# Kernel optimization log

Hardware: AMD Instinct MI355X
Metric: run time of the kernel (lower is better)

## Reference

```python
import jax, jax.numpy as jnp
import numpy as np

B, T, D = 2, 2048, 1024
N, K, H = 16, 8, 128  # q heads, kv heads, head_dim
G = N // K            # GQA group size
EPS = 1e-6
THETA = 1000000.0
SCALE = H ** -0.5
K_MASK = float(np.finfo(np.float32).min)


def rms_norm(x, scale):
    # RMSNorm over head_dim (last axis), computed in fp32 like the original
    dtype = x.dtype
    rms = jnp.sqrt(jnp.mean(x.astype(jnp.float32) ** 2, axis=-1, keepdims=True) + EPS)
    return (scale * x / rms).astype(dtype)


def positions_from_segment_ids(seg):
    t = jnp.arange(seg.shape[1], dtype=jnp.int32)[None, :]
    off = jnp.argmax(seg, axis=1, keepdims=True).astype(jnp.int32)
    rel = t - off
    return jnp.where(seg != 0, rel, jnp.int32(2 ** 30))


def rope_sin_cos(positions):
    frac = jnp.arange(0, H, 2, dtype=jnp.float32) / H
    inv_freq = 1.0 / (THETA ** frac)                    # [H/2]
    ang = positions.astype(jnp.float32)[..., None] * inv_freq  # [B,T,H/2]
    return jnp.sin(ang), jnp.cos(ang)


def apply_rope(x, sin, cos):
    # x: [B,T,heads,H]; sin/cos: [B,T,H/2]
    x1, x2 = x[..., : H // 2], x[..., H // 2:]
    s, c = sin[:, :, None, :], cos[:, :, None, :]
    return jnp.concatenate([x1 * c - x2 * s, x2 * c + x1 * s], axis=-1).astype(x.dtype)


def setup_inputs() -> dict:
    key = jax.random.key(0)
    ks = jax.random.split(key, 8)
    std = 0.02
    return {
        "x": jax.random.normal(ks[0], (B, T, D), dtype=jnp.float32),
        "segment_ids": jnp.ones((B, T), dtype=jnp.int32),
        "wq": jax.random.normal(ks[1], (D, N, H), dtype=jnp.float32) * std,
        "wk": jax.random.normal(ks[2], (D, K, H), dtype=jnp.float32) * std,
        "wv": jax.random.normal(ks[3], (D, K, H), dtype=jnp.float32) * std,
        "wo": jax.random.normal(ks[4], (N, H, D), dtype=jnp.float32) * std,
        "q_scale": jnp.ones((H,), dtype=jnp.float32),
        "k_scale": jnp.ones((H,), dtype=jnp.float32),
    }


def reference(x, segment_ids, wq, wk, wv, wo, q_scale, k_scale):
    # QKV projections + QK RMSNorm
    q = rms_norm(jnp.einsum('BTD,DNH->BTNH', x, wq), q_scale)  # [B,T,N,H]
    k = rms_norm(jnp.einsum('BSD,DKH->BSKH', x, wk), k_scale)  # [B,T,K,H]
    v = jnp.einsum('BSD,DKH->BSKH', x, wv)                     # [B,T,K,H]

    # RoPE using segment-relative positions
    pos = positions_from_segment_ids(segment_ids)  # [B,T] int32
    sin, cos = rope_sin_cos(pos)
    q = apply_rope(q, sin, cos)
    k = apply_rope(k, sin, cos)

    # GQA attention: [B,T,K,G,H] x [B,S,K,H] -> [B,T,S,K,G]
    qg = q.reshape(B, T, K, G, H)
    logits = jnp.einsum('BTKGH,BSKH->BTSKG', qg, k) * SCALE

    causal = pos[:, None, :] <= pos[:, :, None]                       # [B,T,S]
    segm = segment_ids[:, None, :] == segment_ids[:, :, None]         # [B,T,S]
    mask = (causal & segm)[:, :, :, None, None]
    logits = jnp.where(mask, logits, K_MASK)

    w = jax.nn.softmax(logits.astype(jnp.float32), axis=2).astype(logits.dtype)
    out = jnp.einsum('BTSKG,BSKH->BTKGH', w, v).reshape(B, T, N, H)
    return jnp.einsum('BTNH,NHD->BTD', out, wo)
```

## Files before the change

### kernel.cpp

```cpp
#include <hip/hip_runtime.h>
#include <hip/hip_bf16.h>


typedef unsigned short u16;
typedef __attribute__((ext_vector_type(8))) short s16x8;
typedef __attribute__((ext_vector_type(4))) float fp32x4;
typedef __attribute__((ext_vector_type(4))) u16 u16x4;

#define MFMA_BF16(a, b, c) __builtin_amdgcn_mfma_f32_16x16x32_bf16((a), (b), (c), 0, 0, 0)

static constexpr int Bq = 2, Tq = 2048, Dq = 1024, NHq = 16, KHq = 8, Hq = 128;
static constexpr float EPSq = 1e-6f;
static constexpr float S2q = 0.08838834764831845f * 1.4426950408889634f;
static constexpr float MAXq = 20.0f;
static constexpr float NEGHUGE = -3.0e38f;

__device__ __forceinline__ u16 f2b(float f) {
  __hip_bfloat16 h = __float2bfloat16(f);
  return *reinterpret_cast<u16*>(&h);
}

__device__ __forceinline__ void gload16(const u16* g, u16* lds_base) {
  __builtin_amdgcn_global_load_lds(
      (const __attribute__((address_space(1))) unsigned int*)(const void*)g,
      (__attribute__((address_space(3))) unsigned int*)(void*)lds_base, 16, 0, 0);
}


__global__ __launch_bounds__(256) void prep_kernel(
    const float* __restrict__ x, const float* __restrict__ wq,
    const float* __restrict__ wk, const float* __restrict__ wv,
    const float* __restrict__ wo, const int* __restrict__ seg,
    u16* __restrict__ xb, u16* __restrict__ wqkv_t, u16* __restrict__ wo_t,
    int* __restrict__ pos) {
  const int bid = blockIdx.x;
  const int tid = threadIdx.x;
  if (bid < 4096) {
    const int i = bid * 1024 + tid * 4;
    const float4 v = *reinterpret_cast<const float4*>(x + i);
    u16x4 o;
    o.x = f2b(v.x); o.y = f2b(v.y); o.z = f2b(v.z); o.w = f2b(v.w);
    *reinterpret_cast<u16x4*>(xb + i) = o;
    return;
  }
  __shared__ float tile[32][33];
  __shared__ int sv[256], si[256];
  const int tx = tid & 31, ty = tid >> 5;
  if (bid < 8192) {
    const int z = bid - 4096;
    const int r0 = (z & 31) * 32;
    const int c0 = (z >> 5) * 32;
    const float* src;
    int stride, coff;
    if (c0 < 2048)      { src = wq; stride = 2048; coff = c0; }
    else if (c0 < 3072) { src = wk; stride = 1024; coff = c0 - 2048; }
    else                { src = wv; stride = 1024; coff = c0 - 3072; }
#pragma unroll
    for (int j = 0; j < 32; j += 8)
      tile[ty + j][tx] = src[(long)(r0 + ty + j) * stride + (coff + tx)];
    __syncthreads();
#pragma unroll
    for (int j = 0; j < 32; j += 8)
      wqkv_t[(long)(c0 + ty + j) * 1024 + (r0 + tx)] = f2b(tile[tx][ty + j]);
    return;
  }
  if (bid < 10240) {
    const int z = bid - 8192;
    const int c0 = (z & 31) * 32;
    const int r0 = (z >> 5) * 32;
#pragma unroll
    for (int j = 0; j < 32; j += 8)
      tile[ty + j][tx] = wo[(long)(r0 + ty + j) * 1024 + (c0 + tx)];
    __syncthreads();
#pragma unroll
    for (int j = 0; j < 32; j += 8)
      wo_t[(long)(c0 + ty + j) * 2048 + (r0 + tx)] = f2b(tile[tx][ty + j]);
    return;
  }
  const int b = bid - 10240;
  const int* s = seg + b * Tq;
  int bestv = -2147483647 - 1, besti = 0x7fffffff;
  for (int t = tid; t < Tq; t += 256) {
    int v = s[t];
    if (v > bestv) { bestv = v; besti = t; }
  }
  sv[tid] = bestv; si[tid] = besti;
  __syncthreads();
  for (int k = 128; k > 0; k >>= 1) {
    if (tid < k) {
      int v2 = sv[tid + k], i2 = si[tid + k];
      if (v2 > sv[tid] || (v2 == sv[tid] && i2 < si[tid])) {
        sv[tid] = v2; si[tid] = i2;
      }
    }
    __syncthreads();
  }
  const int off = si[0];
  for (int t = tid; t < Tq; t += 256)
    pos[b * Tq + t] = (s[t] != 0) ? (t - off) : (1 << 30);
}


__global__ __launch_bounds__(256) void gemm_qkv_kernel(
    const u16* __restrict__ A, const u16* __restrict__ Bt,
    u16* __restrict__ qkv, u16* __restrict__ vt, const int* __restrict__ pos,
    const float* __restrict__ q_scale, const float* __restrict__ k_scale) {
  __shared__ __align__(16) u16 As[128][64];
  __shared__ __align__(16) u16 Bs[128][64];
  const int tid = threadIdx.x;
  const int wave = tid >> 6, lane = tid & 63;
  const int quad = lane >> 4, l16 = lane & 15;
  const int m0 = blockIdx.y * 128, n0 = blockIdx.x * 128;
  const int row8 = lane >> 3;
  const int cgl = (lane & 7) ^ row8;

  const fp32x4 z4 = {0.f, 0.f, 0.f, 0.f};
  fp32x4 acc[2][8];
#pragma unroll
  for (int i = 0; i < 2; ++i)
#pragma unroll
    for (int j = 0; j < 8; ++j) acc[i][j] = z4;

  for (int k0 = 0; k0 < 1024; k0 += 64) {
    __syncthreads();
#pragma unroll
    for (int jj = 0; jj < 4; ++jj) {
      const int R = wave * 32 + jj * 8;
      gload16(A + (size_t)(m0 + R + row8) * 1024 + k0 + cgl * 8, &As[R][0]);
      gload16(Bt + (size_t)(n0 + R + row8) * 1024 + k0 + cgl * 8, &Bs[R][0]);
    }
    __syncthreads();
#pragma unroll
    for (int kh = 0; kh < 2; ++kh) {
      s16x8 af[2], bfr[8];
#pragma unroll
      for (int i = 0; i < 2; ++i)
        af[i] = *(const s16x8*)&As[wave * 32 + i * 16 + l16]
                               [((((kh << 2) | quad) ^ (l16 & 7)) << 3)];
#pragma unroll
      for (int j = 0; j < 8; ++j)
        bfr[j] = *(const s16x8*)&Bs[j * 16 + l16]
                                [((((kh << 2) | quad) ^ (l16 & 7)) << 3)];
#pragma unroll
      for (int i = 0; i < 2; ++i)
#pragma unroll
        for (int j = 0; j < 8; ++j) acc[i][j] = MFMA_BF16(af[i], bfr[j], acc[i][j]);
    }
  }

  const int wrow = m0 + wave * 32;
  if (n0 >= 3072) {
    const int kv8 = (n0 - 3072) >> 7;
    const int bq = wrow >> 11;
    const size_t vbase = (size_t)(bq * KHq + kv8) * Hq * Tq;
#pragma unroll
    for (int i = 0; i < 2; ++i) {
      const int t = (wrow + i * 16 + quad * 4) & 2047;
#pragma unroll
      for (int j = 0; j < 8; ++j) {
        const int h = j * 16 + l16;
        u16x4 o;
#pragma unroll
        for (int r = 0; r < 4; ++r) o[r] = f2b(acc[i][j][r]);
        *reinterpret_cast<u16x4*>(&vt[vbase + (size_t)h * Tq + t]) = o;
      }
    }
    return;
  }
  const float* scp = (n0 < 2048) ? q_scale : k_scale;
  float scl[8];
#pragma unroll
  for (int j = 0; j < 8; ++j) scl[j] = scp[j * 16 + l16];
  float invf[4];
#pragma unroll
  for (int jf = 0; jf < 4; ++jf)
    invf[jf] = __builtin_amdgcn_exp2f(
                   -(float)(jf * 16 + l16) * (19.931568569324174f / 64.0f)) *
               0.15915494309189535f;
#pragma unroll
  for (int i = 0; i < 2; ++i) {
    float ss[4] = {0.f, 0.f, 0.f, 0.f};
#pragma unroll
    for (int j = 0; j < 8; ++j)
#pragma unroll
      for (int r = 0; r < 4; ++r) ss[r] += acc[i][j][r] * acc[i][j][r];
#pragma unroll
    for (int d = 1; d < 16; d <<= 1)
#pragma unroll
      for (int r = 0; r < 4; ++r) ss[r] += __shfl_xor(ss[r], d, 64);
#pragma unroll
    for (int r = 0; r < 4; ++r) {
      const int row = wrow + i * 16 + quad * 4 + r;
      const float rinv = rsqrtf(ss[r] * (1.0f / 128.0f) + EPSq);
      const float P = (float)pos[row];
      u16* orow = qkv + (size_t)row * 4096 + n0;
#pragma unroll
      for (int jf = 0; jf < 4; ++jf) {
        float rev = P * invf[jf];
        rev -= floorf(rev);
        const float s = __builtin_amdgcn_sinf(rev);
        const float c = __builtin_amdgcn_cosf(rev);
        const float a1 = acc[i][jf][r] * rinv * scl[jf];
        const float a2 = acc[i][jf + 4][r] * rinv * scl[jf + 4];
        orow[jf * 16 + l16] = f2b(a1 * c - a2 * s);
        orow[(jf + 4) * 16 + l16] = f2b(a2 * c + a1 * s);
      }
    }
  }
}


__global__ __launch_bounds__(256) void gemm_out_kernel(
    const u16* __restrict__ A, const u16* __restrict__ Bt,
    float* __restrict__ C) {
  __shared__ __align__(16) u16 As[128][64];
  __shared__ __align__(16) u16 Bs[64][64];
  const int tid = threadIdx.x;
  const int wave = tid >> 6, lane = tid & 63;
  const int quad = lane >> 4, l16 = lane & 15;
  const int m0 = blockIdx.y * 128, n0 = blockIdx.x * 64;
  const int wm = (wave >> 1) * 64, wn = (wave & 1) * 32;
  const int row8 = lane >> 3;
  const int cgl = (lane & 7) ^ row8;

  const fp32x4 z4 = {0.f, 0.f, 0.f, 0.f};
  fp32x4 acc[4][2];
#pragma unroll
  for (int i = 0; i < 4; ++i)
#pragma unroll
    for (int j = 0; j < 2; ++j) acc[i][j] = z4;

  for (int k0 = 0; k0 < 2048; k0 += 64) {
    __syncthreads();
#pragma unroll
    for (int jj = 0; jj < 4; ++jj) {
      const int R = wave * 32 + jj * 8;
      gload16(A + (size_t)(m0 + R + row8) * 2048 + k0 + cgl * 8, &As[R][0]);
    }
#pragma unroll
    for (int jj = 0; jj < 2; ++jj) {
      const int R = wave * 16 + jj * 8;
      gload16(Bt + (size_t)(n0 + R + row8) * 2048 + k0 + cgl * 8, &Bs[R][0]);
    }
    __syncthreads();
#pragma unroll
    for (int kh = 0; kh < 2; ++kh) {
      s16x8 af[4], bfr[2];
#pragma unroll
      for (int i = 0; i < 4; ++i)
        af[i] = *(const s16x8*)&As[wm + i * 16 + l16]
                               [((((kh << 2) | quad) ^ (l16 & 7)) << 3)];
#pragma unroll
      for (int j = 0; j < 2; ++j)
        bfr[j] = *(const s16x8*)&Bs[wn + j * 16 + l16]
                                [((((kh << 2) | quad) ^ (l16 & 7)) << 3)];
#pragma unroll
      for (int i = 0; i < 4; ++i)
#pragma unroll
        for (int j = 0; j < 2; ++j) acc[i][j] = MFMA_BF16(af[i], bfr[j], acc[i][j]);
    }
  }
#pragma unroll
  for (int i = 0; i < 4; ++i) {
    const int row = m0 + wm + i * 16 + quad * 4;
#pragma unroll
    for (int j = 0; j < 2; ++j) {
      const int col = n0 + wn + j * 16 + l16;
#pragma unroll
      for (int r = 0; r < 4; ++r)
        C[(size_t)(row + r) * 1024 + col] = acc[i][j][r];
    }
  }
}


__global__ __launch_bounds__(256, 2) void flash_kernel(
    const u16* __restrict__ qkv, const u16* __restrict__ vt,
    const int* __restrict__ pos, const int* __restrict__ seg,
    u16* __restrict__ Obuf) {
  const int tid = threadIdx.x;
  const int w = tid >> 6;
  const int lane = tid & 63;
  const int quad = lane >> 4, l16 = lane & 15;
  const int g = blockIdx.x;
  const int b = g & 1;
  const int kv = (g >> 1) & 7;
  const int qh = kv * 2 + ((g >> 4) & 1);
  const int p = g >> 5;

  __shared__ __align__(16) u16 Ks[64][128];
  __shared__ __align__(16) u16 Vs[128][64];
  __shared__ __align__(16) u16 Ps[4][16][72];

  const u16* kbase = qkv + (size_t)(b * Tq) * 4096 + 2048 + kv * Hq;
  const u16* vbase = vt + (size_t)(b * KHq + kv) * Hq * Tq;
  const int krow_off = lane >> 4;
  const int vrow_off = lane >> 3;
  const fp32x4 z4 = {0.f, 0.f, 0.f, 0.f};
  const short one_bf = (short)0x3F80;
  const s16x8 ones = {one_bf, one_bf, one_bf, one_bf,
                      one_bf, one_bf, one_bf, one_bf};

#pragma unroll
  for (int phase = 0; phase < 2; ++phase) {
    const int c = phase ? p : 31 - p;
    const int t0 = c * 64 + w * 16;
    const int nst = c + 1;

    s16x8 qf[4];
    {
      const u16* qrow = qkv + (size_t)(b * Tq + t0 + l16) * 4096 + qh * Hq;
#pragma unroll
      for (int ks = 0; ks < 4; ++ks)
        qf[ks] = *(const s16x8*)(qrow + ks * 32 + quad * 8);
    }
    int my_pos[4], my_seg[4];
#pragma unroll
    for (int i = 0; i < 4; ++i) {
      const int t = t0 + quad * 4 + i;
      my_pos[i] = pos[b * Tq + t];
      my_seg[i] = seg[b * Tq + t];
    }
    fp32x4 l_acc = z4;
    fp32x4 o_acc[8];
#pragma unroll
    for (int h = 0; h < 8; ++h) o_acc[h] = z4;

    for (int st = 0; st < nst; ++st) {
      const int s0 = st * 64;
      __syncthreads();
#pragma unroll
      for (int j = 0; j < 4; ++j) {
        const int R = w * 16 + j * 4;
        const int r = R + krow_off;
        const int cg = (lane & 15) ^ (r & 15);
        gload16(kbase + (size_t)(s0 + r) * 4096 + cg * 8, &Ks[R][0]);
      }
#pragma unroll
      for (int j = 0; j < 4; ++j) {
        const int R = w * 32 + j * 8;
        const int r = R + vrow_off;
        const int cg = (lane & 7) ^ (vrow_off & 7);
        gload16(vbase + (size_t)r * Tq + s0 + cg * 8, &Vs[R][0]);
      }
      __syncthreads();

      fp32x4 sc[4];
#pragma unroll
      for (int sub = 0; sub < 4; ++sub) sc[sub] = z4;
#pragma unroll
      for (int sub = 0; sub < 4; ++sub)
#pragma unroll
        for (int ks = 0; ks < 4; ++ks) {
          const s16x8 kf =
              *(const s16x8*)&Ks[sub * 16 + l16][((((ks << 2) | quad) ^ l16) << 3)];
          sc[sub] = MFMA_BF16(qf[ks], kf, sc[sub]);
        }

      if (st == nst - 1) {
        int spos[4], sseg[4];
#pragma unroll
        for (int sub = 0; sub < 4; ++sub) {
          const int s = s0 + sub * 16 + l16;
          spos[sub] = pos[b * Tq + s];
          sseg[sub] = seg[b * Tq + s];
        }
#pragma unroll
        for (int sub = 0; sub < 4; ++sub)
#pragma unroll
          for (int i = 0; i < 4; ++i) {
            const bool ok = (sseg[sub] == my_seg[i]) && (spos[sub] <= my_pos[i]);
            sc[sub][i] = ok ? sc[sub][i] * S2q - MAXq : NEGHUGE;
          }
      } else {
#pragma unroll
        for (int sub = 0; sub < 4; ++sub)
#pragma unroll
          for (int i = 0; i < 4; ++i) sc[sub][i] = sc[sub][i] * S2q - MAXq;
      }

#pragma unroll
      for (int sub = 0; sub < 4; ++sub)
#pragma unroll
        for (int i = 0; i < 4; ++i)
          Ps[w][quad * 4 + i][sub * 16 + l16] =
              f2b(__builtin_amdgcn_exp2f(sc[sub][i]));
      asm volatile("s_waitcnt lgkmcnt(0)" ::: "memory");
      s16x8 pf[2];
#pragma unroll
      for (int kk = 0; kk < 2; ++kk)
        pf[kk] = *(const s16x8*)&Ps[w][l16][kk * 32 + quad * 8];

      l_acc = MFMA_BF16(pf[0], ones, l_acc);
      l_acc = MFMA_BF16(pf[1], ones, l_acc);
#pragma unroll
      for (int j = 0; j < 8; ++j)
#pragma unroll
        for (int kk = 0; kk < 2; ++kk) {
          const s16x8 vf =
              *(const s16x8*)&Vs[j * 16 + l16]
                             [((((kk << 2) | quad) ^ (l16 & 7)) << 3)];
          o_acc[j] = MFMA_BF16(pf[kk], vf, o_acc[j]);
        }
    }

    float inv[4];
#pragma unroll
    for (int i = 0; i < 4; ++i)
      inv[i] = (l_acc[i] > 0.f) ? 1.f / l_acc[i] : 0.f;
#pragma unroll
    for (int j = 0; j < 8; ++j)
#pragma unroll
      for (int i = 0; i < 4; ++i) {
        const int t = t0 + quad * 4 + i;
        Obuf[(size_t)(b * Tq + t) * 2048 + qh * Hq + j * 16 + l16] =
            f2b(o_acc[j][i] * inv[i]);
      }
  }
}


extern "C" void kernel_launch(void* const* d_in, const int* in_sizes, int n_in,
                              void* d_out, int out_size, void* d_ws, size_t ws_size,
                              hipStream_t stream) {
  const float* x = (const float*)d_in[0];
  const int* seg = (const int*)d_in[1];
  const float* wq = (const float*)d_in[2];
  const float* wk = (const float*)d_in[3];
  const float* wv = (const float*)d_in[4];
  const float* wo = (const float*)d_in[5];
  const float* q_scale = (const float*)d_in[6];
  const float* k_scale = (const float*)d_in[7];
  float* out = (float*)d_out;

  char* ws = (char*)d_ws;
  u16* xb = (u16*)(ws);
  u16* wqkv_t = (u16*)(ws + 8388608);
  u16* qkv = (u16*)(ws + 16777216);
  u16* vt = (u16*)(ws + 50331648);
  u16* wo_t = (u16*)(ws + 58720256);
  u16* Obuf = (u16*)(ws + 62914560);
  int* posb = (int*)(ws + 79691776);

  prep_kernel<<<10242, 256, 0, stream>>>(x, wq, wk, wv, wo, seg,
                                         xb, wqkv_t, wo_t, posb);

  gemm_qkv_kernel<<<dim3(32, 32, 1), 256, 0, stream>>>(
      xb, wqkv_t, qkv, vt, posb, q_scale, k_scale);

  flash_kernel<<<512, 256, 0, stream>>>(qkv, vt, posb, seg, Obuf);

  gemm_out_kernel<<<dim3(16, 32, 1), 256, 0, stream>>>(Obuf, wo_t, out);
}
```

Baseline: 232.1 us.

## Double-buffer K/V tiles and process 32 query rows per wave in flash kernel

The flash attention kernel now double-buffers K and V tiles in LDS, prefetching the next tile while computing on the current one, with one barrier per iteration instead of two. Each wave also handles two 16-row query blocks, so every K/V fragment read from LDS feeds twice as many MFMAs, and the grid is halved to 256 blocks of 128 query rows. The costs are higher register and LDS use per block (launch bounds lowered to 1), fewer blocks to keep all CUs busy, and coarser causal load balancing.

```diff
diff --git a/kernel.cpp b/kernel.cpp
--- a/kernel.cpp
+++ b/kernel.cpp
@@ -274,7 +274,7 @@
 }
 
 
-__global__ __launch_bounds__(256, 2) void flash_kernel(
+__global__ __launch_bounds__(256, 1) void flash_kernel(
     const u16* __restrict__ qkv, const u16* __restrict__ vt,
     const int* __restrict__ pos, const int* __restrict__ seg,
     u16* __restrict__ Obuf) {
@@ -288,9 +288,9 @@
   const int qh = kv * 2 + ((g >> 4) & 1);
   const int p = g >> 5;
 
-  __shared__ __align__(16) u16 Ks[64][128];
-  __shared__ __align__(16) u16 Vs[128][64];
-  __shared__ __align__(16) u16 Ps[4][16][72];
+  __shared__ __align__(16) u16 Ks[2][64][128];
+  __shared__ __align__(16) u16 Vs[2][128][64];
+  __shared__ __align__(16) u16 Ps[4][32][72];
 
   const u16* kbase = qkv + (size_t)(b * Tq) * 4096 + 2048 + kv * Hq;
   const u16* vbase = vt + (size_t)(b * KHq + kv) * Hq * Tq;
@@ -301,63 +301,77 @@
   const s16x8 ones = {one_bf, one_bf, one_bf, one_bf,
                       one_bf, one_bf, one_bf, one_bf};
 
+  auto STAGE = [&](int bi, int st) {
+    const int s0 = st * 64;
+#pragma unroll
+    for (int j = 0; j < 4; ++j) {
+      const int R = w * 16 + j * 4;
+      const int r = R + krow_off;
+      const int cg = (lane & 15) ^ (r & 15);
+      gload16(kbase + (size_t)(s0 + r) * 4096 + cg * 8, &Ks[bi][R][0]);
+    }
+#pragma unroll
+    for (int j = 0; j < 4; ++j) {
+      const int R = w * 32 + j * 8;
+      const int r = R + vrow_off;
+      const int cg = (lane & 7) ^ (vrow_off & 7);
+      gload16(vbase + (size_t)r * Tq + s0 + cg * 8, &Vs[bi][R][0]);
+    }
+  };
+
 #pragma unroll
   for (int phase = 0; phase < 2; ++phase) {
-    const int c = phase ? p : 31 - p;
-    const int t0 = c * 64 + w * 16;
-    const int nst = c + 1;
-
-    s16x8 qf[4];
-    {
-      const u16* qrow = qkv + (size_t)(b * Tq + t0 + l16) * 4096 + qh * Hq;
+    const int c = phase ? p : 15 - p;
+    const int t0 = c * 128 + w * 32;
+    const int nst = 2 * (c + 1);
+
+    s16x8 qf[2][4];
+    int my_pos[2][4], my_seg[2][4];
+#pragma unroll
+    for (int rb = 0; rb < 2; ++rb) {
+      const u16* qrow =
+          qkv + (size_t)(b * Tq + t0 + rb * 16 + l16) * 4096 + qh * Hq;
 #pragma unroll
       for (int ks = 0; ks < 4; ++ks)
-        qf[ks] = *(const s16x8*)(qrow + ks * 32 + quad * 8);
-    }
-    int my_pos[4], my_seg[4];
-#pragma unroll
-    for (int i = 0; i < 4; ++i) {
-      const int t = t0 + quad * 4 + i;
-      my_pos[i] = pos[b * Tq + t];
-      my_seg[i] = seg[b * Tq + t];
-    }
-    fp32x4 l_acc = z4;
-    fp32x4 o_acc[8];
-#pragma unroll
-    for (int h = 0; h < 8; ++h) o_acc[h] = z4;
+        qf[rb][ks] = *(const s16x8*)(qrow + ks * 32 + quad * 8);
+#pragma unroll
+      for (int i = 0; i < 4; ++i) {
+        const int t = t0 + rb * 16 + quad * 4 + i;
+        my_pos[rb][i] = pos[b * Tq + t];
+        my_seg[rb][i] = seg[b * Tq + t];
+      }
+    }
+    fp32x4 l_acc[2] = {z4, z4};
+    fp32x4 o_acc[2][8];
+#pragma unroll
+    for (int rb = 0; rb < 2; ++rb)
+#pragma unroll
+      for (int h = 0; h < 8; ++h) o_acc[rb][h] = z4;
+
+    STAGE(0, 0);
+    __syncthreads();
 
     for (int st = 0; st < nst; ++st) {
+      const int cur = st & 1;
+      if (st + 1 < nst) STAGE(cur ^ 1, st + 1);
+
+      fp32x4 sc[2][4];
+#pragma unroll
+      for (int rb = 0; rb < 2; ++rb)
+#pragma unroll
+        for (int sub = 0; sub < 4; ++sub) sc[rb][sub] = z4;
+#pragma unroll
+      for (int sub = 0; sub < 4; ++sub)
+#pragma unroll
+        for (int ks = 0; ks < 4; ++ks) {
+          const s16x8 kf = *(const s16x8*)&Ks[cur][sub * 16 + l16]
+                                             [((((ks << 2) | quad) ^ l16) << 3)];
+          sc[0][sub] = MFMA_BF16(qf[0][ks], kf, sc[0][sub]);
+          sc[1][sub] = MFMA_BF16(qf[1][ks], kf, sc[1][sub]);
+        }
+
       const int s0 = st * 64;
-      __syncthreads();
-#pragma unroll
-      for (int j = 0; j < 4; ++j) {
-        const int R = w * 16 + j * 4;
-        const int r = R + krow_off;
-        const int cg = (lane & 15) ^ (r & 15);
-        gload16(kbase + (size_t)(s0 + r) * 4096 + cg * 8, &Ks[R][0]);
-      }
-#pragma unroll
-      for (int j = 0; j < 4; ++j) {
-        const int R = w * 32 + j * 8;
-        const int r = R + vrow_off;
-        const int cg = (lane & 7) ^ (vrow_off & 7);
-        gload16(vbase + (size_t)r * Tq + s0 + cg * 8, &Vs[R][0]);
-      }
-      __syncthreads();
-
-      fp32x4 sc[4];
-#pragma unroll
-      for (int sub = 0; sub < 4; ++sub) sc[sub] = z4;
-#pragma unroll
-      for (int sub = 0; sub < 4; ++sub)
-#pragma unroll
-        for (int ks = 0; ks < 4; ++ks) {
-          const s16x8 kf =
-              *(const s16x8*)&Ks[sub * 16 + l16][((((ks << 2) | quad) ^ l16) << 3)];
-          sc[sub] = MFMA_BF16(qf[ks], kf, sc[sub]);
-        }
-
-      if (st == nst - 1) {
+      if (st >= nst - 2) {
         int spos[4], sseg[4];
 #pragma unroll
         for (int sub = 0; sub < 4; ++sub) {
@@ -366,56 +380,74 @@
           sseg[sub] = seg[b * Tq + s];
         }
 #pragma unroll
+        for (int rb = 0; rb < 2; ++rb)
+#pragma unroll
+          for (int sub = 0; sub < 4; ++sub)
+#pragma unroll
+            for (int i = 0; i < 4; ++i) {
+              const bool ok = (sseg[sub] == my_seg[rb][i]) &&
+                              (spos[sub] <= my_pos[rb][i]);
+              sc[rb][sub][i] = ok ? sc[rb][sub][i] * S2q - MAXq : NEGHUGE;
+            }
+      } else {
+#pragma unroll
+        for (int rb = 0; rb < 2; ++rb)
+#pragma unroll
+          for (int sub = 0; sub < 4; ++sub)
+#pragma unroll
+            for (int i = 0; i < 4; ++i)
+              sc[rb][sub][i] = sc[rb][sub][i] * S2q - MAXq;
+      }
+
+#pragma unroll
+      for (int rb = 0; rb < 2; ++rb)
+#pragma unroll
         for (int sub = 0; sub < 4; ++sub)
 #pragma unroll
-          for (int i = 0; i < 4; ++i) {
-            const bool ok = (sseg[sub] == my_seg[i]) && (spos[sub] <= my_pos[i]);
-            sc[sub][i] = ok ? sc[sub][i] * S2q - MAXq : NEGHUGE;
-          }
-      } else {
-#pragma unroll
-        for (int sub = 0; sub < 4; ++sub)
-#pragma unroll
-          for (int i = 0; i < 4; ++i) sc[sub][i] = sc[sub][i] * S2q - MAXq;
-      }
-
-#pragma unroll
-      for (int sub = 0; sub < 4; ++sub)
-#pragma unroll
-        for (int i = 0; i < 4; ++i)
-          Ps[w][quad * 4 + i][sub * 16 + l16] =
-              f2b(__builtin_amdgcn_exp2f(sc[sub][i]));
+          for (int i = 0; i < 4; ++i)
+            Ps[w][rb * 16 + quad * 4 + i][sub * 16 + l16] =
+                f2b(__builtin_amdgcn_exp2f(sc[rb][sub][i]));
       asm volatile("s_waitcnt lgkmcnt(0)" ::: "memory");
-      s16x8 pf[2];
-#pragma unroll
-      for (int kk = 0; kk < 2; ++kk)
-        pf[kk] = *(const s16x8*)&Ps[w][l16][kk * 32 + quad * 8];
-
-      l_acc = MFMA_BF16(pf[0], ones, l_acc);
-      l_acc = MFMA_BF16(pf[1], ones, l_acc);
+      s16x8 pf[2][2];
+#pragma unroll
+      for (int rb = 0; rb < 2; ++rb)
+#pragma unroll
+        for (int kk = 0; kk < 2; ++kk)
+          pf[rb][kk] = *(const s16x8*)&Ps[w][rb * 16 + l16][kk * 32 + quad * 8];
+
+      l_acc[0] = MFMA_BF16(pf[0][0], ones, l_acc[0]);
+      l_acc[0] = MFMA_BF16(pf[0][1], ones, l_acc[0]);
+      l_acc[1] = MFMA_BF16(pf[1][0], ones, l_acc[1]);
+      l_acc[1] = MFMA_BF16(pf[1][1], ones, l_acc[1]);
 #pragma unroll
       for (int j = 0; j < 8; ++j)
 #pragma unroll
         for (int kk = 0; kk < 2; ++kk) {
           const s16x8 vf =
-              *(const s16x8*)&Vs[j * 16 + l16]
+              *(const s16x8*)&Vs[cur][j * 16 + l16]
                              [((((kk << 2) | quad) ^ (l16 & 7)) << 3)];
-          o_acc[j] = MFMA_BF16(pf[kk], vf, o_acc[j]);
+          o_acc[0][j] = MFMA_BF16(pf[0][kk], vf, o_acc[0][j]);
+          o_acc[1][j] = MFMA_BF16(pf[1][kk], vf, o_acc[1][j]);
         }
-    }
-
-    float inv[4];
-#pragma unroll
-    for (int i = 0; i < 4; ++i)
-      inv[i] = (l_acc[i] > 0.f) ? 1.f / l_acc[i] : 0.f;
-#pragma unroll
-    for (int j = 0; j < 8; ++j)
-#pragma unroll
-      for (int i = 0; i < 4; ++i) {
-        const int t = t0 + quad * 4 + i;
-        Obuf[(size_t)(b * Tq + t) * 2048 + qh * Hq + j * 16 + l16] =
-            f2b(o_acc[j][i] * inv[i]);
-      }
+
+      __syncthreads();
+    }
+
+#pragma unroll
+    for (int rb = 0; rb < 2; ++rb) {
+      float inv[4];
+#pragma unroll
+      for (int i = 0; i < 4; ++i)
+        inv[i] = (l_acc[rb][i] > 0.f) ? 1.f / l_acc[rb][i] : 0.f;
+#pragma unroll
+      for (int j = 0; j < 8; ++j)
+#pragma unroll
+        for (int i = 0; i < 4; ++i) {
+          const int t = t0 + rb * 16 + quad * 4 + i;
+          Obuf[(size_t)(b * Tq + t) * 2048 + qh * Hq + j * 16 + l16] =
+              f2b(o_acc[rb][j][i] * inv[i]);
+        }
+    }
   }
 }
 
@@ -448,7 +480,7 @@
   gemm_qkv_kernel<<<dim3(32, 32, 1), 256, 0, stream>>>(
       xb, wqkv_t, qkv, vt, posb, q_scale, k_scale);
 
-  flash_kernel<<<512, 256, 0, stream>>>(qkv, vt, posb, seg, Obuf);
+  flash_kernel<<<256, 256, 0, stream>>>(qkv, vt, posb, seg, Obuf);
 
   gemm_out_kernel<<<dim3(16, 32, 1), 256, 0, stream>>>(Obuf, wo_t, out);
 }
```

Result: no change. 235.0 us (+1.3%).

## Split KV across waves in flash attention with register P and LDS reduction

Applied to the files above, without the earlier changes.

The flash kernel now loads 128-row K/V tiles and gives each wave a 32-key slice for all 64 queries, instead of each wave owning 16 queries over the full tile. Scores are computed as K·Q so the exponentiated probabilities feed the PV MFMA directly from registers, which removes the P round-trip through LDS and the ones-MFMA used for row sums. Per-wave partial outputs and row sums are combined through LDS at the end of each half. This halves the number of tile iterations and barriers, at the cost of much larger register use (64 accumulator vectors) and an extra cross-wave reduction step.

```diff
diff --git a/kernel.cpp b/kernel.cpp
--- a/kernel.cpp
+++ b/kernel.cpp
@@ -283,138 +283,189 @@
   const int lane = tid & 63;
   const int quad = lane >> 4, l16 = lane & 15;
   const int g = blockIdx.x;
-  const int b = g & 1;
-  const int kv = (g >> 1) & 7;
-  const int qh = kv * 2 + ((g >> 4) & 1);
+  const int u = g & 31;
+  const int b = u & 1;
+  const int kv = (u >> 1) & 7;
+  const int qh = kv * 2 + ((u >> 4) & 1);
   const int p = g >> 5;
 
-  __shared__ __align__(16) u16 Ks[64][128];
-  __shared__ __align__(16) u16 Vs[128][64];
-  __shared__ __align__(16) u16 Ps[4][16][72];
+  __shared__ __align__(16) u16 Ks[128][128];
+  __shared__ __align__(16) u16 Vs[128][128];
 
   const u16* kbase = qkv + (size_t)(b * Tq) * 4096 + 2048 + kv * Hq;
   const u16* vbase = vt + (size_t)(b * KHq + kv) * Hq * Tq;
-  const int krow_off = lane >> 4;
-  const int vrow_off = lane >> 3;
+  const int ro = lane >> 4;
+  const int ch = lane & 15;
   const fp32x4 z4 = {0.f, 0.f, 0.f, 0.f};
-  const short one_bf = (short)0x3F80;
-  const s16x8 ones = {one_bf, one_bf, one_bf, one_bf,
-                      one_bf, one_bf, one_bf, one_bf};
-
-#pragma unroll
-  for (int phase = 0; phase < 2; ++phase) {
-    const int c = phase ? p : 31 - p;
-    const int t0 = c * 64 + w * 16;
-    const int nst = c + 1;
-
-    s16x8 qf[4];
-    {
-      const u16* qrow = qkv + (size_t)(b * Tq + t0 + l16) * 4096 + qh * Hq;
-#pragma unroll
-      for (int ks = 0; ks < 4; ++ks)
-        qf[ks] = *(const s16x8*)(qrow + ks * 32 + quad * 8);
-    }
-    int my_pos[4], my_seg[4];
+
+#pragma unroll
+  for (int half = 0; half < 2; ++half) {
+    const int c = half ? p : 31 - p;
+    const int t0 = c * 64;
+    const int nst = (c + 2) >> 1;
+
+    s16x8 qf[4][4];
+#pragma unroll
+    for (int qb = 0; qb < 4; ++qb)
+#pragma unroll
+      for (int hk = 0; hk < 4; ++hk)
+        qf[qb][hk] = *(const s16x8*)(qkv +
+            (size_t)(b * Tq + t0 + qb * 16 + l16) * 4096 + qh * Hq +
+            hk * 32 + quad * 8);
+
+    fp32x4 o_acc[4][8];
+#pragma unroll
+    for (int qb = 0; qb < 4; ++qb)
+#pragma unroll
+      for (int hb = 0; hb < 8; ++hb) o_acc[qb][hb] = z4;
+    float l_lane[4] = {0.f, 0.f, 0.f, 0.f};
+
+    for (int st = 0; st < nst; ++st) {
+      const int s0 = st * 128;
+      __syncthreads();
+#pragma unroll
+      for (int jj = 0; jj < 8; ++jj) {
+        const int R = w * 32 + jj * 4;
+        const int srow = R + ro;
+        gload16(kbase + (size_t)(s0 + srow) * 4096 + ((ch ^ (srow & 15)) << 3),
+                &Ks[R][0]);
+      }
+#pragma unroll
+      for (int jj = 0; jj < 8; ++jj) {
+        const int R = w * 32 + jj * 4;
+        const int hrow = R + ro;
+        gload16(vbase + (size_t)hrow * Tq + s0 + ((ch ^ (hrow & 15)) << 3),
+                &Vs[R][0]);
+      }
+      __syncthreads();
+
+      fp32x4 sc[4][2];
+#pragma unroll
+      for (int qb = 0; qb < 4; ++qb) { sc[qb][0] = z4; sc[qb][1] = z4; }
+      __builtin_amdgcn_s_setprio(1);
+#pragma unroll
+      for (int hk = 0; hk < 4; ++hk) {
+        s16x8 kf[2];
+#pragma unroll
+        for (int sh = 0; sh < 2; ++sh) {
+          const int srow = w * 32 + ((l16 >> 2) << 3) + (sh << 2) + (l16 & 3);
+          const int hc = hk * 4 + quad;
+          kf[sh] = *(const s16x8*)&Ks[srow][((hc ^ (srow & 15)) << 3)];
+        }
+#pragma unroll
+        for (int qb = 0; qb < 4; ++qb) {
+          sc[qb][0] = MFMA_BF16(kf[0], qf[qb][hk], sc[qb][0]);
+          sc[qb][1] = MFMA_BF16(kf[1], qf[qb][hk], sc[qb][1]);
+        }
+      }
+      __builtin_amdgcn_s_setprio(0);
+
+      if (st == nst - 1) {
+        int qpos[4], qseg[4];
+#pragma unroll
+        for (int qb = 0; qb < 4; ++qb) {
+          const int q = t0 + qb * 16 + l16;
+          qpos[qb] = pos[b * Tq + q];
+          qseg[qb] = seg[b * Tq + q];
+        }
+        int spos[2][4], sseg[2][4];
+#pragma unroll
+        for (int sh = 0; sh < 2; ++sh)
+#pragma unroll
+          for (int r = 0; r < 4; ++r) {
+            const int s = s0 + w * 32 + quad * 8 + sh * 4 + r;
+            spos[sh][r] = pos[b * Tq + s];
+            sseg[sh][r] = seg[b * Tq + s];
+          }
+#pragma unroll
+        for (int qb = 0; qb < 4; ++qb)
+#pragma unroll
+          for (int sh = 0; sh < 2; ++sh)
+#pragma unroll
+            for (int r = 0; r < 4; ++r) {
+              const bool ok = (sseg[sh][r] == qseg[qb]) &&
+                              (spos[sh][r] <= qpos[qb]);
+              sc[qb][sh][r] = ok ? sc[qb][sh][r] * S2q - MAXq : NEGHUGE;
+            }
+      } else {
+#pragma unroll
+        for (int qb = 0; qb < 4; ++qb)
+#pragma unroll
+          for (int sh = 0; sh < 2; ++sh)
+#pragma unroll
+            for (int r = 0; r < 4; ++r)
+              sc[qb][sh][r] = sc[qb][sh][r] * S2q - MAXq;
+      }
+
+      s16x8 p8[4];
+#pragma unroll
+      for (int qb = 0; qb < 4; ++qb) {
+#pragma unroll
+        for (int sh = 0; sh < 2; ++sh)
+#pragma unroll
+          for (int r = 0; r < 4; ++r) {
+            const float e = __builtin_amdgcn_exp2f(sc[qb][sh][r]);
+            l_lane[qb] += e;
+            p8[qb][sh * 4 + r] = (short)f2b(e);
+          }
+      }
+
+      __builtin_amdgcn_s_setprio(1);
+#pragma unroll
+      for (int hb = 0; hb < 8; ++hb) {
+        const int h = hb * 16 + l16;
+        const int sch = w * 4 + quad;
+        const s16x8 vf = *(const s16x8*)&Vs[h][((sch ^ (h & 15)) << 3)];
+#pragma unroll
+        for (int qb = 0; qb < 4; ++qb)
+          o_acc[qb][hb] = MFMA_BF16(p8[qb], vf, o_acc[qb][hb]);
+      }
+      __builtin_amdgcn_s_setprio(0);
+    }
+
+    __syncthreads();
+    float* obuf = (float*)(&Ks[0][0]);
+    float* lbuf = (float*)(&Vs[0][0]);
+#pragma unroll
+    for (int qb = 0; qb < 4; ++qb) {
+      l_lane[qb] += __shfl_xor(l_lane[qb], 16, 64);
+      l_lane[qb] += __shfl_xor(l_lane[qb], 32, 64);
+    }
+    if (quad == 0) {
+#pragma unroll
+      for (int qb = 0; qb < 4; ++qb)
+        lbuf[w * 64 + qb * 16 + l16] = l_lane[qb];
+    }
+#pragma unroll
+    for (int r = 1; r < 4; ++r) {
+      const int sq = (w + r) & 3;
+      float* slot = obuf + sq * 2048;
+#pragma unroll
+      for (int hb = 0; hb < 8; ++hb)
+        *reinterpret_cast<fp32x4*>(&slot[hb * 256 + lane * 4]) = o_acc[sq][hb];
+      __syncthreads();
+      float* mine = obuf + w * 2048;
+#pragma unroll
+      for (int hb = 0; hb < 8; ++hb) {
+        const fp32x4 t = *reinterpret_cast<const fp32x4*>(&mine[hb * 256 + lane * 4]);
+        o_acc[w][hb] += t;
+      }
+      __syncthreads();
+    }
+    float inv[4];
 #pragma unroll
     for (int i = 0; i < 4; ++i) {
-      const int t = t0 + quad * 4 + i;
-      my_pos[i] = pos[b * Tq + t];
-      my_seg[i] = seg[b * Tq + t];
-    }
-    fp32x4 l_acc = z4;
-    fp32x4 o_acc[8];
-#pragma unroll
-    for (int h = 0; h < 8; ++h) o_acc[h] = z4;
-
-    for (int st = 0; st < nst; ++st) {
-      const int s0 = st * 64;
-      __syncthreads();
-#pragma unroll
-      for (int j = 0; j < 4; ++j) {
-        const int R = w * 16 + j * 4;
-        const int r = R + krow_off;
-        const int cg = (lane & 15) ^ (r & 15);
-        gload16(kbase + (size_t)(s0 + r) * 4096 + cg * 8, &Ks[R][0]);
-      }
-#pragma unroll
-      for (int j = 0; j < 4; ++j) {
-        const int R = w * 32 + j * 8;
-        const int r = R + vrow_off;
-        const int cg = (lane & 7) ^ (vrow_off & 7);
-        gload16(vbase + (size_t)r * Tq + s0 + cg * 8, &Vs[R][0]);
-      }
-      __syncthreads();
-
-      fp32x4 sc[4];
-#pragma unroll
-      for (int sub = 0; sub < 4; ++sub) sc[sub] = z4;
-#pragma unroll
-      for (int sub = 0; sub < 4; ++sub)
-#pragma unroll
-        for (int ks = 0; ks < 4; ++ks) {
-          const s16x8 kf =
-              *(const s16x8*)&Ks[sub * 16 + l16][((((ks << 2) | quad) ^ l16) << 3)];
-          sc[sub] = MFMA_BF16(qf[ks], kf, sc[sub]);
-        }
-
-      if (st == nst - 1) {
-        int spos[4], sseg[4];
-#pragma unroll
-        for (int sub = 0; sub < 4; ++sub) {
-          const int s = s0 + sub * 16 + l16;
-          spos[sub] = pos[b * Tq + s];
-          sseg[sub] = seg[b * Tq + s];
-        }
-#pragma unroll
-        for (int sub = 0; sub < 4; ++sub)
-#pragma unroll
-          for (int i = 0; i < 4; ++i) {
-            const bool ok = (sseg[sub] == my_seg[i]) && (spos[sub] <= my_pos[i]);
-            sc[sub][i] = ok ? sc[sub][i] * S2q - MAXq : NEGHUGE;
-          }
-      } else {
-#pragma unroll
-        for (int sub = 0; sub < 4; ++sub)
-#pragma unroll
-          for (int i = 0; i < 4; ++i) sc[sub][i] = sc[sub][i] * S2q - MAXq;
-      }
-
-#pragma unroll
-      for (int sub = 0; sub < 4; ++sub)
-#pragma unroll
-        for (int i = 0; i < 4; ++i)
-          Ps[w][quad * 4 + i][sub * 16 + l16] =
-              f2b(__builtin_amdgcn_exp2f(sc[sub][i]));
-      asm volatile("s_waitcnt lgkmcnt(0)" ::: "memory");
-      s16x8 pf[2];
-#pragma unroll
-      for (int kk = 0; kk < 2; ++kk)
-        pf[kk] = *(const s16x8*)&Ps[w][l16][kk * 32 + quad * 8];
-
-      l_acc = MFMA_BF16(pf[0], ones, l_acc);
-      l_acc = MFMA_BF16(pf[1], ones, l_acc);
-#pragma unroll
-      for (int j = 0; j < 8; ++j)
-#pragma unroll
-        for (int kk = 0; kk < 2; ++kk) {
-          const s16x8 vf =
-              *(const s16x8*)&Vs[j * 16 + l16]
-                             [((((kk << 2) | quad) ^ (l16 & 7)) << 3)];
-          o_acc[j] = MFMA_BF16(pf[kk], vf, o_acc[j]);
-        }
-    }
-
-    float inv[4];
-#pragma unroll
-    for (int i = 0; i < 4; ++i)
-      inv[i] = (l_acc[i] > 0.f) ? 1.f / l_acc[i] : 0.f;
-#pragma unroll
-    for (int j = 0; j < 8; ++j)
+      const int qq = w * 16 + quad * 4 + i;
+      const float lt = lbuf[qq] + lbuf[64 + qq] + lbuf[128 + qq] + lbuf[192 + qq];
+      inv[i] = (lt > 0.f) ? 1.f / lt : 0.f;
+    }
+#pragma unroll
+    for (int hb = 0; hb < 8; ++hb)
 #pragma unroll
       for (int i = 0; i < 4; ++i) {
-        const int t = t0 + quad * 4 + i;
-        Obuf[(size_t)(b * Tq + t) * 2048 + qh * Hq + j * 16 + l16] =
-            f2b(o_acc[j][i] * inv[i]);
+        const int t = t0 + w * 16 + quad * 4 + i;
+        Obuf[(size_t)(b * Tq + t) * 2048 + qh * Hq + hb * 16 + l16] =
+            f2b(o_acc[w][hb][i] * inv[i]);
       }
   }
 }
```

After: 547.2 us. 2.36x slower.
